# Kernel tuning notes

Measured on AMD Instinct MI355X. Metric: run time of the kernel, lower is better.

Reference implementation:

```python
import jax, jax.numpy as jnp
import numpy as np

N = 100000   # nodes
E = 3200000  # edges
G = 2048     # graphs in batch
F_IN, H, EXTRA = 9, 64, 32
EPS = 1e-5


def setup_inputs() -> dict:
    key = jax.random.key(0)
    ks = jax.random.split(key, 24)
    w = lambda k, s: (jax.random.normal(k, s, jnp.float32) * 0.05)
    inp = {
        "x": jax.random.normal(ks[0], (N, F_IN), jnp.float32),
        "edge_index": jax.random.randint(ks[1], (2, E), 0, N),
        "batch": jnp.sort(jax.random.randint(ks[2], (N,), 0, G)),
        "extra": jax.random.normal(ks[3], (G, EXTRA), jnp.float32),
        # GCN layer params
        "W1": w(ks[4], (F_IN, H)), "b1": jnp.zeros((H,), jnp.float32),
        "W2": w(ks[5], (H, H)),    "b2": jnp.zeros((H,), jnp.float32),
        "W3": w(ks[6], (H, H)),    "b3": jnp.zeros((H,), jnp.float32),
        # MLP: [H+EXTRA, 128, 64, 32, 1]
        "Wm0": w(ks[7], (H + EXTRA, 128)), "bm0": jnp.zeros((128,), jnp.float32),
        "g0": jnp.ones((128,), jnp.float32), "be0": jnp.zeros((128,), jnp.float32),
        "Wm1": w(ks[8], (128, 64)), "bm1": jnp.zeros((64,), jnp.float32),
        "g1": jnp.ones((64,), jnp.float32), "be1": jnp.zeros((64,), jnp.float32),
        "Wm2": w(ks[9], (64, 32)), "bm2": jnp.zeros((32,), jnp.float32),
        "g2": jnp.ones((32,), jnp.float32), "be2": jnp.zeros((32,), jnp.float32),
        "Wm3": w(ks[10], (32, 1)), "bm3": jnp.zeros((1,), jnp.float32),
    }
    return inp


def reference(x, edge_index, batch, extra,
              W1, b1, W2, b2, W3, b3,
              Wm0, bm0, g0, be0, Wm1, bm1, g1, be1,
              Wm2, bm2, g2, be2, Wm3, bm3):
    n = x.shape[0]
    # GCN normalization (PyG gcn_norm with self-loops)
    loops = jnp.arange(n)
    src = jnp.concatenate([edge_index[0], loops])
    dst = jnp.concatenate([edge_index[1], loops])
    deg = jax.ops.segment_sum(jnp.ones_like(dst, jnp.float32), dst, num_segments=n)
    dis = jnp.where(deg > 0, jax.lax.rsqrt(deg), 0.0)
    coef = (dis[src] * dis[dst])[:, None]  # [E+N, 1]

    def gcn(h, W, b):
        h = h @ W                                         # transform first (as PyG)
        agg = jax.ops.segment_sum(h[src] * coef, dst, num_segments=n)
        return agg + b

    h = jax.nn.relu(gcn(x, W1, b1))
    h = jax.nn.relu(gcn(h, W2, b2))
    h = jax.nn.relu(gcn(h, W3, b3))

    # global mean pool over graphs
    cnt = jax.ops.segment_sum(jnp.ones((n,), jnp.float32), batch, num_segments=G)
    emb = jax.ops.segment_sum(h, batch, num_segments=G) / jnp.maximum(cnt, 1.0)[:, None]

    z = jnp.concatenate([emb, extra], axis=1)  # [G, H+EXTRA]

    def bn(h, g, b):  # BatchNorm1d, training-mode batch stats
        mu = h.mean(0)
        var = h.var(0)
        return (h - mu) * jax.lax.rsqrt(var + EPS) * g + b

    z = jax.nn.relu(bn(z @ Wm0 + bm0, g0, be0))
    z = jax.nn.relu(bn(z @ Wm1 + bm1, g1, be1))
    z = jax.nn.relu(bn(z @ Wm2 + bm2, g2, be2))
    return (z @ Wm3 + bm3).reshape(-1)  # [G]
```

## Files before the change

kernel.cpp:

```cpp
#include <hip/hip_runtime.h>

#define NN 100000
#define NE 3200000
#define NG 2048
#define FIN 9
#define HD 64
#define XD 32
#define BN_EPS 1e-5f
#define CAP 96
#define NBUCK 1024
#define BNODES 98
#define ECAP 3840
#define P1_CHUNK 16384

__device__ __forceinline__ unsigned f2bf(float f) {
    unsigned u = __float_as_uint(f);
    return (u + 0x7fffu + ((u >> 16) & 1u)) >> 16;
}
__device__ __forceinline__ unsigned pack2bf(float lo, float hi) {
    return f2bf(lo) | (f2bf(hi) << 16);
}
__device__ __forceinline__ float bflo(unsigned u) { return __uint_as_float(u << 16); }
__device__ __forceinline__ float bfhi(unsigned u) { return __uint_as_float(u & 0xffff0000u); }

__global__ void k_zeroi(int* p, int n) {
    int i = blockIdx.x * 256 + threadIdx.x;
    if (i < n) p[i] = 0;
}

__global__ __launch_bounds__(256) void k_split(const int* __restrict__ src,
                                               const int* __restrict__ dst,
                                               int* __restrict__ gcur,
                                               unsigned* __restrict__ ebuf) {
    __shared__ int hcnt[NBUCK];
    __shared__ int hbase[NBUCK];
    int tid = threadIdx.x;
    long e0 = (long)blockIdx.x * P1_CHUNK;
    long e1 = e0 + P1_CHUNK;
    if (e1 > NE) e1 = NE;
    for (int b = tid; b < NBUCK; b += 256) hcnt[b] = 0;
    __syncthreads();
    for (long e = e0 + tid; e < e1; e += 256) {
        int d = dst[e];
        atomicAdd(&hcnt[d / BNODES], 1);
    }
    __syncthreads();
    for (int b = tid; b < NBUCK; b += 256) {
        int c = hcnt[b];
        hbase[b] = (c > 0) ? atomicAdd(&gcur[b], c) : 0;
        hcnt[b] = 0;
    }
    __syncthreads();
    for (long e = e0 + tid; e < e1; e += 256) {
        int d = dst[e];
        int s = src[e];
        int b = d / BNODES;
        int dl = d - b * BNODES;
        int pos = hbase[b] + atomicAdd(&hcnt[b], 1);
        if (pos < ECAP)
            ebuf[(long)b * ECAP + pos] = ((unsigned)dl << 17) | (unsigned)s;
    }
}

__global__ __launch_bounds__(256) void k_build(const int* __restrict__ gcur,
                                               const unsigned* __restrict__ ebuf,
                                               int* __restrict__ srcs,
                                               int* __restrict__ deg,
                                               float* __restrict__ dis) {
    __shared__ int lcnt[BNODES];
    __shared__ int lists[BNODES * CAP];
    int b = blockIdx.x;
    int tid = threadIdx.x;
    for (int i = tid; i < BNODES; i += 256) lcnt[i] = 0;
    __syncthreads();
    int cntb = gcur[b];
    if (cntb > ECAP) cntb = ECAP;
    const unsigned* eb = ebuf + (long)b * ECAP;
    for (int t = tid; t < cntb; t += 256) {
        unsigned p = eb[t];
        int dl = p >> 17;
        int s = p & 0x1FFFF;
        int k = atomicAdd(&lcnt[dl], 1);
        if (k < CAP) lists[dl * CAP + k] = s;
    }
    __syncthreads();
    long base = (long)b * BNODES * CAP;
    for (int i = tid; i < BNODES * CAP; i += 256)
        srcs[base + i] = lists[i];
    for (int i = tid; i < BNODES; i += 256) {
        int node = b * BNODES + i;
        if (node < NN) {
            int d = min(lcnt[i], CAP);
            deg[node] = d;
            dis[node] = rsqrtf((float)d + 1.0f);
        }
    }
}


__global__ void k_padx16(const float* __restrict__ x, const float* __restrict__ dis,
                         unsigned* __restrict__ xpd) {
    int gtid = blockIdx.x * 256 + threadIdx.x;
    if (gtid >= NN * 8) return;
    int i = gtid >> 3, u = gtid & 7;
    float d = dis[i];
    int f0 = 2 * u, f1 = 2 * u + 1;
    float a = (f0 < FIN) ? d * x[i * FIN + f0] : 0.f;
    float b = (f1 < FIN) ? d * x[i * FIN + f1] : 0.f;
    xpd[gtid] = pack2bf(a, b);
}

__global__ __launch_bounds__(256) void k_gather_x8(const unsigned* __restrict__ xpd,
                                                   const int* __restrict__ deg,
                                                   const int* __restrict__ srcs,
                                                   const float* __restrict__ dis,
                                                   float* __restrict__ aggx) {
    int tid = threadIdx.x;
    int i = blockIdx.x * 32 + (tid >> 3);
    int lane = tid & 7;
    if (i >= NN) return;
    float di = dis[i];
    unsigned u = xpd[i * 8 + lane];
    float a0 = bflo(u), a1 = bfhi(u);
    int beg = i * CAP, end = beg + deg[i];
    int j = beg;
    for (; j + 3 < end; j += 4) {
        int s0 = srcs[j], s1 = srcs[j + 1], s2 = srcs[j + 2], s3 = srcs[j + 3];
        unsigned u0 = xpd[s0 * 8 + lane];
        unsigned u1 = xpd[s1 * 8 + lane];
        unsigned u2 = xpd[s2 * 8 + lane];
        unsigned u3 = xpd[s3 * 8 + lane];
        a0 += bflo(u0) + bflo(u1) + bflo(u2) + bflo(u3);
        a1 += bfhi(u0) + bfhi(u1) + bfhi(u2) + bfhi(u3);
    }
    for (; j < end; ++j) {
        int s0 = srcs[j];
        unsigned u0 = xpd[s0 * 8 + lane];
        a0 += bflo(u0);
        a1 += bfhi(u0);
    }
    float2 r = make_float2(di * a0, di * a1);
    *reinterpret_cast<float2*>(aggx + (long)i * 16 + lane * 2) = r;
}

__global__ void k_xform9(const float* __restrict__ aggx, const float* __restrict__ W,
                         const float* __restrict__ b, float* __restrict__ out) {
    __shared__ float Ws[FIN * HD];
    int t = threadIdx.x;
    if (t < FIN * HD) Ws[t] = W[t];
    __syncthreads();
    long gtid = (long)blockIdx.x * 256 + t;
    int i = (int)(gtid >> 6);
    int f = (int)(gtid & 63);
    if (i >= NN) return;
    const float* row = aggx + (long)i * 16;
    float acc = b[f];
#pragma unroll
    for (int k = 0; k < FIN; ++k) acc += row[k] * Ws[k * HD + f];
    out[gtid] = acc > 0.f ? acc : 0.f;
}


__global__ void k_xform64d(const float* __restrict__ h, const float* __restrict__ W,
                           const float* __restrict__ dis, unsigned* __restrict__ out16) {
    __shared__ float Ws[HD * HD];
    int t = threadIdx.x;
    for (int k = t; k < HD * HD; k += 256) Ws[k] = W[k];
    __syncthreads();
    long gtid = (long)blockIdx.x * 256 + t;
    int i = (int)(gtid >> 5);
    int u = (int)(gtid & 31);
    if (i >= NN) return;
    const float* row = h + (long)i * HD;
    int f0 = 2 * u;
    float a0 = 0.f, a1 = 0.f;
#pragma unroll
    for (int k = 0; k < HD; ++k) {
        float r = row[k];
        a0 += r * Ws[k * HD + f0];
        a1 += r * Ws[k * HD + f0 + 1];
    }
    float d = dis[i];
    out16[gtid] = pack2bf(d * a0, d * a1);
}

template <int POOL>
__global__ __launch_bounds__(256) void k_gather64b(const unsigned* __restrict__ hWd,
                                                   const int* __restrict__ deg,
                                                   const int* __restrict__ srcs,
                                                   const float* __restrict__ dis,
                                                   const float* __restrict__ b,
                                                   const int* __restrict__ batch,
                                                   float* __restrict__ z,
                                                   float* __restrict__ out) {
    int tid = threadIdx.x;
    int i = blockIdx.x * 8 + (tid >> 5);
    int lane = tid & 31;
    if (i >= NN) return;
    float di = dis[i];
    unsigned u = hWd[(long)i * 32 + lane];
    float a0 = bflo(u), a1 = bfhi(u);
    int beg = i * CAP, end = beg + deg[i];
    int j = beg;
    int s0 = 0, s1 = 0, s2 = 0, s3 = 0;
    if (j + 3 < end) {
        s0 = srcs[j]; s1 = srcs[j + 1]; s2 = srcs[j + 2]; s3 = srcs[j + 3];
    }
    for (; j + 7 < end; j += 4) {
        int t0 = srcs[j + 4], t1 = srcs[j + 5], t2 = srcs[j + 6], t3 = srcs[j + 7];
        unsigned u0 = hWd[(long)s0 * 32 + lane];
        unsigned u1 = hWd[(long)s1 * 32 + lane];
        unsigned u2 = hWd[(long)s2 * 32 + lane];
        unsigned u3 = hWd[(long)s3 * 32 + lane];
        a0 += bflo(u0) + bflo(u1) + bflo(u2) + bflo(u3);
        a1 += bfhi(u0) + bfhi(u1) + bfhi(u2) + bfhi(u3);
        s0 = t0; s1 = t1; s2 = t2; s3 = t3;
    }
    if (j + 3 < end) {
        unsigned u0 = hWd[(long)s0 * 32 + lane];
        unsigned u1 = hWd[(long)s1 * 32 + lane];
        unsigned u2 = hWd[(long)s2 * 32 + lane];
        unsigned u3 = hWd[(long)s3 * 32 + lane];
        a0 += bflo(u0) + bflo(u1) + bflo(u2) + bflo(u3);
        a1 += bfhi(u0) + bfhi(u1) + bfhi(u2) + bfhi(u3);
        j += 4;
    }
    for (; j < end; ++j) {
        int s = srcs[j];
        unsigned u0 = hWd[(long)s * 32 + lane];
        a0 += bflo(u0);
        a1 += bfhi(u0);
    }
    int f0 = 2 * lane;
    float v0 = di * a0 + b[f0];
    float v1 = di * a1 + b[f0 + 1];
    v0 = v0 > 0.f ? v0 : 0.f;
    v1 = v1 > 0.f ? v1 : 0.f;
    if (POOL) {
        int g = batch[i];
        atomicAdd(&z[(long)g * (HD + XD) + f0], v0);
        atomicAdd(&z[(long)g * (HD + XD) + f0 + 1], v1);
    } else {
        *reinterpret_cast<float2*>(out + (long)i * HD + f0) = make_float2(v0, v1);
    }
}


__global__ void k_zero(float* p, long n) {
    long i = (long)blockIdx.x * 256 + threadIdx.x;
    if (i < n) p[i] = 0.f;
}

__global__ void k_cnt(const int* __restrict__ batch, float* __restrict__ cnt) {
    int i = blockIdx.x * 256 + threadIdx.x;
    if (i < NN) atomicAdd(&cnt[batch[i]], 1.0f);
}

__global__ void k_zfin(float* z, const float* __restrict__ cnt,
                       const float* __restrict__ extra) {
    int gtid = blockIdx.x * 256 + threadIdx.x;
    if (gtid >= NG * (HD + XD)) return;
    int g = gtid / (HD + XD);
    int f = gtid % (HD + XD);
    if (f < HD)
        z[gtid] = z[gtid] / fmaxf(cnt[g], 1.0f);
    else
        z[gtid] = extra[g * XD + (f - HD)];
}

template <int K, int M>
__global__ void k_mm(const float* __restrict__ in, const float* __restrict__ W,
                     const float* __restrict__ b, float* __restrict__ out) {
    int gtid = blockIdx.x * 256 + threadIdx.x;
    if (gtid >= NG * M) return;
    int g = gtid / M;
    int m = gtid % M;
    const float* row = in + (long)g * K;
    float acc = b[m];
#pragma unroll 8
    for (int k = 0; k < K; ++k) acc += row[k] * W[k * M + m];
    out[gtid] = acc;
}

template <int M>
__global__ void k_bn_relu(float* z, const float* __restrict__ gamma,
                          const float* __restrict__ beta) {
    int c = blockIdx.x;
    int t = threadIdx.x;
    __shared__ float s1[256], s2[256];
    float sum = 0.f, sumsq = 0.f;
    for (int g = t; g < NG; g += 256) {
        float v = z[(long)g * M + c];
        sum += v;
        sumsq += v * v;
    }
    s1[t] = sum;
    s2[t] = sumsq;
    __syncthreads();
    for (int o = 128; o > 0; o >>= 1) {
        if (t < o) {
            s1[t] += s1[t + o];
            s2[t] += s2[t + o];
        }
        __syncthreads();
    }
    float mean = s1[0] / (float)NG;
    float var = s2[0] / (float)NG - mean * mean;
    float scale = rsqrtf(var + BN_EPS) * gamma[c];
    float shift = beta[c] - mean * scale;
    for (int g = t; g < NG; g += 256) {
        float v = z[(long)g * M + c] * scale + shift;
        z[(long)g * M + c] = v > 0.f ? v : 0.f;
    }
}

__global__ void k_final(const float* __restrict__ z2, const float* __restrict__ W,
                        const float* __restrict__ b, float* __restrict__ out) {
    int g = blockIdx.x * 256 + threadIdx.x;
    if (g >= NG) return;
    const float* row = z2 + (long)g * 32;
    float acc = b[0];
#pragma unroll
    for (int k = 0; k < 32; ++k) acc += row[k] * W[k];
    out[g] = acc;
}

extern "C" void kernel_launch(void* const* d_in, const int* in_sizes, int n_in,
                              void* d_out, int out_size, void* d_ws, size_t ws_size,
                              hipStream_t stream) {
    const float* x = (const float*)d_in[0];
    const int* ei = (const int*)d_in[1];
    const int* batch = (const int*)d_in[2];
    const float* extra = (const float*)d_in[3];
    const float* W1 = (const float*)d_in[4];
    const float* b1 = (const float*)d_in[5];
    const float* W2 = (const float*)d_in[6];
    const float* b2 = (const float*)d_in[7];
    const float* W3 = (const float*)d_in[8];
    const float* b3 = (const float*)d_in[9];
    const float* Wm0 = (const float*)d_in[10];
    const float* bm0 = (const float*)d_in[11];
    const float* g0 = (const float*)d_in[12];
    const float* be0 = (const float*)d_in[13];
    const float* Wm1 = (const float*)d_in[14];
    const float* bm1 = (const float*)d_in[15];
    const float* g1 = (const float*)d_in[16];
    const float* be1 = (const float*)d_in[17];
    const float* Wm2 = (const float*)d_in[18];
    const float* bm2 = (const float*)d_in[19];
    const float* g2 = (const float*)d_in[20];
    const float* be2 = (const float*)d_in[21];
    const float* Wm3 = (const float*)d_in[22];
    const float* bm3 = (const float*)d_in[23];

    const int* src = ei;
    const int* dst = ei + NE;

    int* deg = (int*)d_ws;
    int* gcur = deg + 100352;
    int* srcs = gcur + 2048;
    float* dis = (float*)(srcs + (long)100352 * CAP);
    unsigned* xpd = (unsigned*)(dis + 100352);
    float* A = (float*)(xpd + (long)NN * 8);
    unsigned* B16 = (unsigned*)(A + (long)NN * HD);
    float* aggx = (float*)B16;
    unsigned* ebuf = (unsigned*)A;
    float* z = (float*)(B16 + (long)NN * 32);
    float* cnt = z + NG * (HD + XD);
    float* t0 = cnt + NG;
    float* t1 = t0 + NG * 128;
    float* t2 = t1 + NG * 64;

    unsigned bN = (NN + 255) / 256;
    unsigned bN32 = (NN * 32 + 255) / 256;
    unsigned bN64 = (NN * 64 + 255) / 256;
    unsigned bG8 = (NN + 7) / 8;

    k_zeroi<<<(NBUCK + 255) / 256, 256, 0, stream>>>(gcur, NBUCK);
    k_split<<<(NE + P1_CHUNK - 1) / P1_CHUNK, 256, 0, stream>>>(src, dst, gcur, ebuf);
    k_build<<<NBUCK, 256, 0, stream>>>(gcur, ebuf, srcs, deg, dis);

    long zlen = (long)NG * (HD + XD) + NG;
    k_zero<<<(unsigned)((zlen + 255) / 256), 256, 0, stream>>>(z, zlen);

    k_padx16<<<(NN * 8 + 255) / 256, 256, 0, stream>>>(x, dis, xpd);
    k_gather_x8<<<(NN + 31) / 32, 256, 0, stream>>>(xpd, deg, srcs, dis, aggx);
    k_xform9<<<bN64, 256, 0, stream>>>(aggx, W1, b1, A);

    k_xform64d<<<bN32, 256, 0, stream>>>(A, W2, dis, B16);
    k_gather64b<0><<<bG8, 256, 0, stream>>>(B16, deg, srcs, dis, b2, batch, z, A);

    k_xform64d<<<bN32, 256, 0, stream>>>(A, W3, dis, B16);
    k_gather64b<1><<<bG8, 256, 0, stream>>>(B16, deg, srcs, dis, b3, batch, z, A);

    k_cnt<<<bN, 256, 0, stream>>>(batch, cnt);
    k_zfin<<<(NG * (HD + XD) + 255) / 256, 256, 0, stream>>>(z, cnt, extra);

    k_mm<96, 128><<<(NG * 128 + 255) / 256, 256, 0, stream>>>(z, Wm0, bm0, t0);
    k_bn_relu<128><<<128, 256, 0, stream>>>(t0, g0, be0);
    k_mm<128, 64><<<(NG * 64 + 255) / 256, 256, 0, stream>>>(t0, Wm1, bm1, t1);
    k_bn_relu<64><<<64, 256, 0, stream>>>(t1, g1, be1);
    k_mm<64, 32><<<(NG * 32 + 255) / 256, 256, 0, stream>>>(t1, Wm2, bm2, t2);
    k_bn_relu<32><<<32, 256, 0, stream>>>(t2, g2, be2);
    k_final<<<(NG + 255) / 256, 256, 0, stream>>>(t2, Wm3, bm3, (float*)d_out);
}
```

Measured before the change: 461.8 us.

## Store hidden activations in bf16, fuse MLP matmul with batchnorm, prefetch x-gather indices

Several changes at once. Intermediate node features between the GCN layers are stored as packed bf16 instead of fp32, which halves activation traffic. The graph-level MLP now keeps activations in a feature-major layout and fuses each matmul with its BatchNorm+ReLU in one kernel, one block per output channel, removing three launches and the extra passes over memory. The first-layer gather prefetches the next group of source indices, as the later layers already did. Rounding to bf16 adds some precision loss in the layer-1 and layer-2 outputs.

```diff
diff --git a/kernel.cpp b/kernel.cpp
--- a/kernel.cpp
+++ b/kernel.cpp
@@ -124,18 +124,32 @@
     float a0 = bflo(u), a1 = bfhi(u);
     int beg = i * CAP, end = beg + deg[i];
     int j = beg;
-    for (; j + 3 < end; j += 4) {
-        int s0 = srcs[j], s1 = srcs[j + 1], s2 = srcs[j + 2], s3 = srcs[j + 3];
+    int s0 = 0, s1 = 0, s2 = 0, s3 = 0;
+    if (j + 3 < end) {
+        s0 = srcs[j]; s1 = srcs[j + 1]; s2 = srcs[j + 2]; s3 = srcs[j + 3];
+    }
+    for (; j + 7 < end; j += 4) {
+        int t0 = srcs[j + 4], t1 = srcs[j + 5], t2 = srcs[j + 6], t3 = srcs[j + 7];
         unsigned u0 = xpd[s0 * 8 + lane];
         unsigned u1 = xpd[s1 * 8 + lane];
         unsigned u2 = xpd[s2 * 8 + lane];
         unsigned u3 = xpd[s3 * 8 + lane];
         a0 += bflo(u0) + bflo(u1) + bflo(u2) + bflo(u3);
         a1 += bfhi(u0) + bfhi(u1) + bfhi(u2) + bfhi(u3);
+        s0 = t0; s1 = t1; s2 = t2; s3 = t3;
+    }
+    if (j + 3 < end) {
+        unsigned u0 = xpd[s0 * 8 + lane];
+        unsigned u1 = xpd[s1 * 8 + lane];
+        unsigned u2 = xpd[s2 * 8 + lane];
+        unsigned u3 = xpd[s3 * 8 + lane];
+        a0 += bflo(u0) + bflo(u1) + bflo(u2) + bflo(u3);
+        a1 += bfhi(u0) + bfhi(u1) + bfhi(u2) + bfhi(u3);
+        j += 4;
     }
     for (; j < end; ++j) {
-        int s0 = srcs[j];
-        unsigned u0 = xpd[s0 * 8 + lane];
+        int s = srcs[j];
+        unsigned u0 = xpd[s * 8 + lane];
         a0 += bflo(u0);
         a1 += bfhi(u0);
     }
@@ -144,24 +158,31 @@
 }
 
 __global__ void k_xform9(const float* __restrict__ aggx, const float* __restrict__ W,
-                         const float* __restrict__ b, float* __restrict__ out) {
+                         const float* __restrict__ b, unsigned* __restrict__ out16) {
     __shared__ float Ws[FIN * HD];
     int t = threadIdx.x;
     if (t < FIN * HD) Ws[t] = W[t];
     __syncthreads();
     long gtid = (long)blockIdx.x * 256 + t;
-    int i = (int)(gtid >> 6);
-    int f = (int)(gtid & 63);
+    int i = (int)(gtid >> 5);
+    int u = (int)(gtid & 31);
     if (i >= NN) return;
     const float* row = aggx + (long)i * 16;
-    float acc = b[f];
-#pragma unroll
-    for (int k = 0; k < FIN; ++k) acc += row[k] * Ws[k * HD + f];
-    out[gtid] = acc > 0.f ? acc : 0.f;
-}
-
-
-__global__ void k_xform64d(const float* __restrict__ h, const float* __restrict__ W,
+    int f0 = 2 * u;
+    float acc0 = b[f0], acc1 = b[f0 + 1];
+#pragma unroll
+    for (int k = 0; k < FIN; ++k) {
+        float r = row[k];
+        acc0 += r * Ws[k * HD + f0];
+        acc1 += r * Ws[k * HD + f0 + 1];
+    }
+    acc0 = acc0 > 0.f ? acc0 : 0.f;
+    acc1 = acc1 > 0.f ? acc1 : 0.f;
+    out16[gtid] = pack2bf(acc0, acc1);
+}
+
+
+__global__ void k_xform64d(const unsigned* __restrict__ h16, const float* __restrict__ W,
                            const float* __restrict__ dis, unsigned* __restrict__ out16) {
     __shared__ float Ws[HD * HD];
     int t = threadIdx.x;
@@ -171,14 +192,15 @@
     int i = (int)(gtid >> 5);
     int u = (int)(gtid & 31);
     if (i >= NN) return;
-    const float* row = h + (long)i * HD;
+    const unsigned* row = h16 + (long)i * 32;
     int f0 = 2 * u;
     float a0 = 0.f, a1 = 0.f;
 #pragma unroll
-    for (int k = 0; k < HD; ++k) {
-        float r = row[k];
-        a0 += r * Ws[k * HD + f0];
-        a1 += r * Ws[k * HD + f0 + 1];
+    for (int k2 = 0; k2 < 32; ++k2) {
+        unsigned w = row[k2];
+        float r0 = bflo(w), r1 = bfhi(w);
+        a0 += r0 * Ws[(2 * k2) * HD + f0] + r1 * Ws[(2 * k2 + 1) * HD + f0];
+        a1 += r0 * Ws[(2 * k2) * HD + f0 + 1] + r1 * Ws[(2 * k2 + 1) * HD + f0 + 1];
     }
     float d = dis[i];
     out16[gtid] = pack2bf(d * a0, d * a1);
@@ -191,8 +213,8 @@
                                                    const float* __restrict__ dis,
                                                    const float* __restrict__ b,
                                                    const int* __restrict__ batch,
-                                                   float* __restrict__ z,
-                                                   float* __restrict__ out) {
+                                                   float* __restrict__ zT,
+                                                   unsigned* __restrict__ out16) {
     int tid = threadIdx.x;
     int i = blockIdx.x * 8 + (tid >> 5);
     int lane = tid & 31;
@@ -238,10 +260,10 @@
     v1 = v1 > 0.f ? v1 : 0.f;
     if (POOL) {
         int g = batch[i];
-        atomicAdd(&z[(long)g * (HD + XD) + f0], v0);
-        atomicAdd(&z[(long)g * (HD + XD) + f0 + 1], v1);
+        atomicAdd(&zT[(long)f0 * NG + g], v0);
+        atomicAdd(&zT[(long)(f0 + 1) * NG + g], v1);
     } else {
-        *reinterpret_cast<float2*>(out + (long)i * HD + f0) = make_float2(v0, v1);
+        out16[(long)i * 32 + lane] = pack2bf(v0, v1);
     }
 }
 
@@ -256,46 +278,45 @@
     if (i < NN) atomicAdd(&cnt[batch[i]], 1.0f);
 }
 
-__global__ void k_zfin(float* z, const float* __restrict__ cnt,
+__global__ void k_zfin(float* zT, const float* __restrict__ cnt,
                        const float* __restrict__ extra) {
     int gtid = blockIdx.x * 256 + threadIdx.x;
-    if (gtid >= NG * (HD + XD)) return;
-    int g = gtid / (HD + XD);
-    int f = gtid % (HD + XD);
+    if (gtid >= (HD + XD) * NG) return;
+    int f = gtid >> 11;
+    int g = gtid & (NG - 1);
     if (f < HD)
-        z[gtid] = z[gtid] / fmaxf(cnt[g], 1.0f);
+        zT[gtid] = zT[gtid] / fmaxf(cnt[g], 1.0f);
     else
-        z[gtid] = extra[g * XD + (f - HD)];
+        zT[gtid] = extra[g * XD + (f - HD)];
 }
 
 template <int K, int M>
-__global__ void k_mm(const float* __restrict__ in, const float* __restrict__ W,
-                     const float* __restrict__ b, float* __restrict__ out) {
-    int gtid = blockIdx.x * 256 + threadIdx.x;
-    if (gtid >= NG * M) return;
-    int g = gtid / M;
-    int m = gtid % M;
-    const float* row = in + (long)g * K;
-    float acc = b[m];
-#pragma unroll 8
-    for (int k = 0; k < K; ++k) acc += row[k] * W[k * M + m];
-    out[gtid] = acc;
-}
-
-template <int M>
-__global__ void k_bn_relu(float* z, const float* __restrict__ gamma,
-                          const float* __restrict__ beta) {
+__global__ __launch_bounds__(256) void k_mmbn(const float* __restrict__ inT,
+                                              const float* __restrict__ W,
+                                              const float* __restrict__ b,
+                                              const float* __restrict__ gamma,
+                                              const float* __restrict__ beta,
+                                              float* __restrict__ outT) {
+    __shared__ float s1[256], s2[256];
     int c = blockIdx.x;
     int t = threadIdx.x;
-    __shared__ float s1[256], s2[256];
-    float sum = 0.f, sumsq = 0.f;
-    for (int g = t; g < NG; g += 256) {
-        float v = z[(long)g * M + c];
-        sum += v;
-        sumsq += v * v;
-    }
-    s1[t] = sum;
-    s2[t] = sumsq;
+    float acc[NG / 256];
+#pragma unroll
+    for (int r = 0; r < NG / 256; ++r) acc[r] = b[c];
+    for (int k = 0; k < K; ++k) {
+        float w = W[k * M + c];
+        const float* row = inT + (long)k * NG;
+#pragma unroll
+        for (int r = 0; r < NG / 256; ++r) acc[r] += row[r * 256 + t] * w;
+    }
+    float s = 0.f, ss = 0.f;
+#pragma unroll
+    for (int r = 0; r < NG / 256; ++r) {
+        s += acc[r];
+        ss += acc[r] * acc[r];
+    }
+    s1[t] = s;
+    s2[t] = ss;
     __syncthreads();
     for (int o = 128; o > 0; o >>= 1) {
         if (t < o) {
@@ -308,20 +329,20 @@
     float var = s2[0] / (float)NG - mean * mean;
     float scale = rsqrtf(var + BN_EPS) * gamma[c];
     float shift = beta[c] - mean * scale;
-    for (int g = t; g < NG; g += 256) {
-        float v = z[(long)g * M + c] * scale + shift;
-        z[(long)g * M + c] = v > 0.f ? v : 0.f;
-    }
-}
-
-__global__ void k_final(const float* __restrict__ z2, const float* __restrict__ W,
+#pragma unroll
+    for (int r = 0; r < NG / 256; ++r) {
+        float v = acc[r] * scale + shift;
+        outT[(long)c * NG + r * 256 + t] = v > 0.f ? v : 0.f;
+    }
+}
+
+__global__ void k_final(const float* __restrict__ t2T, const float* __restrict__ W,
                         const float* __restrict__ b, float* __restrict__ out) {
     int g = blockIdx.x * 256 + threadIdx.x;
     if (g >= NG) return;
-    const float* row = z2 + (long)g * 32;
     float acc = b[0];
 #pragma unroll
-    for (int k = 0; k < 32; ++k) acc += row[k] * W[k];
+    for (int k = 0; k < 32; ++k) acc += t2T[(long)k * NG + g] * W[k];
     out[g] = acc;
 }
 
@@ -361,46 +382,42 @@
     int* srcs = gcur + 2048;
     float* dis = (float*)(srcs + (long)100352 * CAP);
     unsigned* xpd = (unsigned*)(dis + 100352);
-    float* A = (float*)(xpd + (long)NN * 8);
-    unsigned* B16 = (unsigned*)(A + (long)NN * HD);
+    unsigned* A16 = xpd + (long)NN * 8;
+    unsigned* B16 = A16 + (long)NN * 32;
     float* aggx = (float*)B16;
-    unsigned* ebuf = (unsigned*)A;
-    float* z = (float*)(B16 + (long)NN * 32);
-    float* cnt = z + NG * (HD + XD);
-    float* t0 = cnt + NG;
-    float* t1 = t0 + NG * 128;
-    float* t2 = t1 + NG * 64;
+    unsigned* ebuf = A16;
+    float* zT = (float*)(B16 + (long)NN * 32);
+    float* cnt = zT + (HD + XD) * NG;
+    float* t0T = cnt + NG;
+    float* t1T = t0T + 128 * NG;
+    float* t2T = t1T + 64 * NG;
 
     unsigned bN = (NN + 255) / 256;
     unsigned bN32 = (NN * 32 + 255) / 256;
-    unsigned bN64 = (NN * 64 + 255) / 256;
     unsigned bG8 = (NN + 7) / 8;
 
     k_zeroi<<<(NBUCK + 255) / 256, 256, 0, stream>>>(gcur, NBUCK);
     k_split<<<(NE + P1_CHUNK - 1) / P1_CHUNK, 256, 0, stream>>>(src, dst, gcur, ebuf);
     k_build<<<NBUCK, 256, 0, stream>>>(gcur, ebuf, srcs, deg, dis);
 
-    long zlen = (long)NG * (HD + XD) + NG;
-    k_zero<<<(unsigned)((zlen + 255) / 256), 256, 0, stream>>>(z, zlen);
+    long zlen = (long)(HD + XD) * NG + NG;
+    k_zero<<<(unsigned)((zlen + 255) / 256), 256, 0, stream>>>(zT, zlen);
 
     k_padx16<<<(NN * 8 + 255) / 256, 256, 0, stream>>>(x, dis, xpd);
     k_gather_x8<<<(NN + 31) / 32, 256, 0, stream>>>(xpd, deg, srcs, dis, aggx);
-    k_xform9<<<bN64, 256, 0, stream>>>(aggx, W1, b1, A);
-
-    k_xform64d<<<bN32, 256, 0, stream>>>(A, W2, dis, B16);
-    k_gather64b<0><<<bG8, 256, 0, stream>>>(B16, deg, srcs, dis, b2, batch, z, A);
-
-    k_xform64d<<<bN32, 256, 0, stream>>>(A, W3, dis, B16);
-    k_gather64b<1><<<bG8, 256, 0, stream>>>(B16, deg, srcs, dis, b3, batch, z, A);
+    k_xform9<<<bN32, 256, 0, stream>>>(aggx, W1, b1, A16);
+
+    k_xform64d<<<bN32, 256, 0, stream>>>(A16, W2, dis, B16);
+    k_gather64b<0><<<bG8, 256, 0, stream>>>(B16, deg, srcs, dis, b2, batch, zT, A16);
+
+    k_xform64d<<<bN32, 256, 0, stream>>>(A16, W3, dis, B16);
+    k_gather64b<1><<<bG8, 256, 0, stream>>>(B16, deg, srcs, dis, b3, batch, zT, A16);
 
     k_cnt<<<bN, 256, 0, stream>>>(batch, cnt);
-    k_zfin<<<(NG * (HD + XD) + 255) / 256, 256, 0, stream>>>(z, cnt, extra);
-
-    k_mm<96, 128><<<(NG * 128 + 255) / 256, 256, 0, stream>>>(z, Wm0, bm0, t0);
-    k_bn_relu<128><<<128, 256, 0, stream>>>(t0, g0, be0);
-    k_mm<128, 64><<<(NG * 64 + 255) / 256, 256, 0, stream>>>(t0, Wm1, bm1, t1);
-    k_bn_relu<64><<<64, 256, 0, stream>>>(t1, g1, be1);
-    k_mm<64, 32><<<(NG * 32 + 255) / 256, 256, 0, stream>>>(t1, Wm2, bm2, t2);
-    k_bn_relu<32><<<32, 256, 0, stream>>>(t2, g2, be2);
-    k_final<<<(NG + 255) / 256, 256, 0, stream>>>(t2, Wm3, bm3, (float*)d_out);
-}
+    k_zfin<<<((HD + XD) * NG + 255) / 256, 256, 0, stream>>>(zT, cnt, extra);
+
+    k_mmbn<96, 128><<<128, 256, 0, stream>>>(zT, Wm0, bm0, g0, be0, t0T);
+    k_mmbn<128, 64><<<64, 256, 0, stream>>>(t0T, Wm1, bm1, g1, be1, t1T);
+    k_mmbn<64, 32><<<32, 256, 0, stream>>>(t1T, Wm2, bm2, g2, be2, t2T);
+    k_final<<<(NG + 255) / 256, 256, 0, stream>>>(t2T, Wm3, bm3, (float*)d_out);
+}
```

After: 878.9 us. 90.3% more time.
